# Performance work log

Measured on AMD Instinct MI355X. Metric: run time of the kernel, lower is better.

Reference implementation:

```python
import jax, jax.numpy as jnp
import numpy as np

B, D, I, H, K = 1024, 128, 64, 256, 8
HE = 2 * H  # encoder cell width (mu || log_sigma2)


def setup_inputs() -> dict:
    key = jax.random.key(0)
    ks = jax.random.split(key, 20)
    g = lambda i, shape, s=0.05: jax.random.normal(ks[i], shape, dtype=jnp.float32) * s
    return dict(
        X=g(0, (B, D, I), 1.0),
        W=jax.random.randint(ks[1], (B, D, I), 0, 2).astype(jnp.int32),
        noise=g(2, (B, H), 1.0),
        A=g(3, (D, I)),  # imputation template (learned)
        enc_Wx=g(4, (I, 4 * HE)), enc_Wh=g(5, (HE, 4 * HE)), enc_b=jnp.zeros((4 * HE,), jnp.float32),
        enc_pi=g(6, (HE,)), enc_pf=g(7, (HE,)), enc_po=g(8, (HE,)),
        dec_Wx=g(9, (I, 4 * H)), dec_Wh=g(10, (H, 4 * H)), dec_b=jnp.zeros((4 * H,), jnp.float32),
        dec_pi=g(11, (H,)), dec_pf=g(12, (H,)), dec_po=g(13, (H,)),
        out_w=g(14, (H, I)), out_b=jnp.full((I,), 0.1, jnp.float32),
        mu_c_unscaled=g(15, (K, H)), sigma2_c_unscaled=g(16, (K, H)), phi_c_unscaled=g(17, (K,)),
    )


def peephole_lstm(x_seq, Wx, Wh, b, pi, pf, po, h0, c0):
    """Keras PeepholeLSTMCell, gate order i,f,c,o. x_seq: [T,B,I] -> (hs [T,B,n], hT, cT)."""
    def step(carry, x):
        h, c = carry
        z = x @ Wx + h @ Wh + b
        zi, zf, zc, zo = jnp.split(z, 4, axis=-1)
        i = jax.nn.sigmoid(zi + pi * c)
        f = jax.nn.sigmoid(zf + pf * c)
        c_new = f * c + i * jnp.tanh(zc)
        o = jax.nn.sigmoid(zo + po * c_new)
        h_new = o * jnp.tanh(c_new)
        return (h_new, c_new), h_new
    (hT, cT), hs = jax.lax.scan(step, (h0, c0), x_seq)
    return hs, hT, cT


def reference(X, W, noise, A, enc_Wx, enc_Wh, enc_b, enc_pi, enc_pf, enc_po,
              dec_Wx, dec_Wh, dec_b, dec_pi, dec_pf, dec_po,
              out_w, out_b, mu_c_unscaled, sigma2_c_unscaled, phi_c_unscaled):
    Bn = X.shape[0]
    Wf = W.astype(X.dtype)
    X_imp = X * Wf + A * (1.0 - Wf)  # masked imputation
    # --- encode: peephole LSTM, take FINAL CELL STATE (encoder_rnn(...)[-1]) ---
    x_seq = jnp.swapaxes(X_imp, 0, 1)  # [D,B,I]
    h0 = jnp.zeros((Bn, HE), X.dtype)
    _, _, cT = peephole_lstm(x_seq, enc_Wx, enc_Wh, enc_b, enc_pi, enc_pf, enc_po, h0, h0)
    mu_tilde = cT[:, :H]
    log_sigma2_tilde = cT[:, H:]
    z = mu_tilde + jnp.exp(0.5 * log_sigma2_tilde) * noise
    # --- decode: zero inputs, initial_state = (h=0, c=z) ---
    dec_in = jnp.zeros((D, Bn, I), X.dtype)
    hs, _, _ = peephole_lstm(dec_in, dec_Wx, dec_Wh, dec_b, dec_pi, dec_pf, dec_po,
                             jnp.zeros((Bn, H), X.dtype), z)
    rnn_out = jnp.swapaxes(hs, 0, 1)  # [B,D,H]
    x_raw = rnn_out @ out_w + out_b   # [B,D,I]
    x = jax.nn.sigmoid(x_raw)
    # --- GMM parameters ---
    mu_c = mu_c_unscaled
    sigma2_c = jax.nn.softplus(sigma2_c_unscaled)
    phi_c = jax.nn.softmax(phi_c_unscaled)
    return (x, x_raw, mu_c, sigma2_c, phi_c, z, mu_tilde, log_sigma2_tilde)
```

## Files before the change

### kernel.cpp

```cpp
#include <hip/hip_runtime.h>
#include <hip/hip_bf16.h>

typedef __attribute__((ext_vector_type(4))) float f32x4;
typedef __attribute__((ext_vector_type(8))) short bf16x8;

#define NB 1024
#define ND 128
#define NI 64
#define NH 256
#define NHE 512
#define KENC 576
#define NENC 2048
#define KDEC 256
#define ESTR 584
#define DSTR 264

__device__ __forceinline__ float sigmf(float x) { return 1.0f / (1.0f + __expf(-x)); }
__device__ __forceinline__ float tanh_f(float x) { return 1.0f - 2.0f / (__expf(2.0f * x) + 1.0f); }

__device__ __forceinline__ f32x4 mfma16(bf16x8 a, bf16x8 b, f32x4 c) {
    return __builtin_amdgcn_mfma_f32_16x16x32_bf16(a, b, c, 0, 0, 0);
}

__device__ __forceinline__ void st_ull(unsigned long long* p, unsigned long long v) {
    __hip_atomic_store(p, v, __ATOMIC_RELAXED, __HIP_MEMORY_SCOPE_AGENT);
}
__device__ __forceinline__ unsigned long long ld_ull(const unsigned long long* p) {
    return __hip_atomic_load(p, __ATOMIC_RELAXED, __HIP_MEMORY_SCOPE_AGENT);
}
__device__ __forceinline__ void st_flag(int* p) {
    __hip_atomic_store(p, 1, __ATOMIC_RELAXED, __HIP_MEMORY_SCOPE_AGENT);
}

__device__ __forceinline__ void wspin(const int* flags, int n, int lane, const int* extra) {
    int g = 0;
    for (;;) {
        int v = 1;
        if (lane < n)
            v = __hip_atomic_load(flags + lane, __ATOMIC_RELAXED, __HIP_MEMORY_SCOPE_AGENT);
        else if (extra != nullptr && lane == n)
            v = __hip_atomic_load(extra, __ATOMIC_RELAXED, __HIP_MEMORY_SCOPE_AGENT);
        if (__all(v != 0)) return;
        __builtin_amdgcn_s_sleep(1);
        if (++g > (1 << 20)) return;
    }
}

__device__ __forceinline__ void quadtr(f32x4 a, int lane,
                                       float& z0, float& z1, float& z2, float& z3) {
    float x0 = a[0], x1 = a[1], x2 = a[2], x3 = a[3];
    float s0 = __shfl_xor(x0, 1), s1 = __shfl_xor(x1, 1),
          s2 = __shfl_xor(x2, 1), s3 = __shfl_xor(x3, 1);
    bool o1 = (lane & 1) != 0;
    float y0 = o1 ? s1 : x0;
    float y1 = o1 ? x1 : s0;
    float y2 = o1 ? s3 : x2;
    float y3 = o1 ? x3 : s2;
    float t0 = __shfl_xor(y0, 2), t1 = __shfl_xor(y1, 2),
          t2 = __shfl_xor(y2, 2), t3 = __shfl_xor(y3, 2);
    bool o2 = (lane & 2) != 0;
    z0 = o2 ? t2 : y0;
    z1 = o2 ? t3 : y1;
    z2 = o2 ? y2 : t0;
    z3 = o2 ? y3 : t1;
}


__global__ void pack_enc_kernel(const float* __restrict__ Wx, const float* __restrict__ Wh,
                                const float* __restrict__ bsrc,
                                __hip_bfloat16* __restrict__ Wp, float* __restrict__ bp)
{
    int n = blockIdx.y;
    int k = blockIdx.x * 256 + threadIdx.x;
    int j = n >> 2, g = n & 3;
    int col = g * NHE + j;
    if (k < KENC) {
        float v = (k < NI) ? Wx[k * NENC + col] : Wh[(k - NI) * NENC + col];
        Wp[(size_t)n * KENC + k] = __float2bfloat16(v);
    }
    if (blockIdx.x == 0 && threadIdx.x == 0) bp[n] = bsrc[col];
}

__global__ void pack_dec_kernel(const float* __restrict__ Wh, const float* __restrict__ ow,
                                const float* __restrict__ bsrc,
                                __hip_bfloat16* __restrict__ Wp, float* __restrict__ bp)
{
    int n = blockIdx.y;
    int k = threadIdx.x;
    float v;
    if (n < 1024) {
        int j = n >> 2, g = n & 3;
        int col = g * NH + j;
        v = Wh[k * 1024 + col];
        if (k == 0) bp[n] = bsrc[col];
    } else if (n < 1088) {
        v = ow[k * NI + (n - 1024)];
    } else {
        v = 0.0f;
    }
    Wp[(size_t)n * KDEC + k] = __float2bfloat16(v);
}

__global__ void pack_xb_kernel(const float* __restrict__ X, const int* __restrict__ W,
                               const float* __restrict__ A, __hip_bfloat16* __restrict__ Xb)
{
    int idx = blockIdx.x * 256 + threadIdx.x;
    int i = idx & 63;
    int t1 = idx >> 6;
    int b = t1 & 1023;
    int d = t1 >> 10;
    int src = (b * ND + d) * NI + i;
    float v = W[src] ? X[src] : A[d * NI + i];
    Xb[idx] = __float2bfloat16(v);
}

__global__ __launch_bounds__(256, 2) void enc_persist(
    const __hip_bfloat16* __restrict__ Xb,
    __hip_bfloat16* __restrict__ h0buf, __hip_bfloat16* __restrict__ h1buf,
    float* __restrict__ cenc,
    const __hip_bfloat16* __restrict__ Wp, const float* __restrict__ bp,
    const float* __restrict__ pi, const float* __restrict__ pf, const float* __restrict__ po,
    int* __restrict__ encfl)
{
    __shared__ __align__(16) unsigned short Alds[32][ESTR];
    __shared__ __align__(16) unsigned short Hlds[32][36];

    const int tid  = threadIdx.x;
    const int lane = tid & 63;
    const int wv   = tid >> 6;
    const int bm   = blockIdx.x;
    const int bn   = blockIdx.y;
    const int m0   = bm * 32;
    const int lr   = lane & 15;
    const int q    = lane >> 4;
    const int lk   = q * 8;

    bf16x8 breg[2][18];
    #pragma unroll
    for (int ni = 0; ni < 2; ++ni) {
        const __hip_bfloat16* wb = Wp + (size_t)(bn * 128 + wv * 32 + ni * 16 + lr) * KENC + lk;
        #pragma unroll
        for (int i = 0; i < 18; ++i)
            breg[ni][i] = *reinterpret_cast<const bf16x8*>(wb + i * 32);
    }

    const int u = lr >> 2;
    const int e = lane & 3;
    float4 bb[2];
    float ppi[2], ppf[2], ppo[2];
    int jl[2];
    #pragma unroll
    for (int ni = 0; ni < 2; ++ni) {
        jl[ni] = wv * 8 + ni * 4 + u;
        int jg = bn * 32 + jl[ni];
        bb[ni] = *reinterpret_cast<const float4*>(bp + 4 * jg);
        ppi[ni] = pi[jg]; ppf[ni] = pf[jg]; ppo[ni] = po[jg];
    }
    const int rowb = 4 * q + e;

    float creg[2][2] = {{0.f, 0.f}, {0.f, 0.f}};
    __hip_bfloat16* hbuf[2] = {h0buf, h1buf};

    for (int t = 0; t < ND; ++t) {
        {
            int row = tid >> 3, ch = tid & 7;
            *reinterpret_cast<bf16x8*>(&Alds[row][ch * 8]) =
                *reinterpret_cast<const bf16x8*>(Xb + ((size_t)t * NB + m0 + row) * NI + ch * 8);
        }
        __syncthreads();

        f32x4 acc[2][2];
        #pragma unroll
        for (int mi = 0; mi < 2; ++mi)
            #pragma unroll
            for (int ni = 0; ni < 2; ++ni) acc[mi][ni] = {0.f, 0.f, 0.f, 0.f};
        #pragma unroll
        for (int i = 0; i < 2; ++i) {
            bf16x8 a[2];
            #pragma unroll
            for (int mi = 0; mi < 2; ++mi)
                a[mi] = *reinterpret_cast<const bf16x8*>(&Alds[16 * mi + lr][i * 32 + lk]);
            #pragma unroll
            for (int mi = 0; mi < 2; ++mi)
                #pragma unroll
                for (int ni = 0; ni < 2; ++ni)
                    acc[mi][ni] = mfma16(a[mi], breg[ni][i], acc[mi][ni]);
        }

        if (t > 0) wspin(encfl + (size_t)(bm * ND + (t - 1)) * 16, 16, lane, nullptr);

        {
            const unsigned long long* hsrc =
                (const unsigned long long*)(hbuf[t & 1] + (size_t)m0 * NHE);
            #pragma unroll
            for (int it = 0; it < 16; ++it) {
                int idx = tid + it * 256;
                int row = idx >> 7, c8 = idx & 127;
                unsigned long long v = ld_ull(hsrc + (size_t)row * 128 + c8);
                *reinterpret_cast<unsigned long long*>(&Alds[row][64 + c8 * 4]) = v;
            }
        }
        __syncthreads();

        #pragma unroll
        for (int i = 2; i < 18; ++i) {
            bf16x8 a[2];
            #pragma unroll
            for (int mi = 0; mi < 2; ++mi)
                a[mi] = *reinterpret_cast<const bf16x8*>(&Alds[16 * mi + lr][i * 32 + lk]);
            #pragma unroll
            for (int mi = 0; mi < 2; ++mi)
                #pragma unroll
                for (int ni = 0; ni < 2; ++ni)
                    acc[mi][ni] = mfma16(a[mi], breg[ni][i], acc[mi][ni]);
        }

        #pragma unroll
        for (int mi = 0; mi < 2; ++mi) {
            #pragma unroll
            for (int ni = 0; ni < 2; ++ni) {
                float z0, z1, z2, z3;
                quadtr(acc[mi][ni], lane, z0, z1, z2, z3);
                float c_old = creg[mi][ni];
                float gi = sigmf(z0 + bb[ni].x + ppi[ni] * c_old);
                float gf = sigmf(z1 + bb[ni].y + ppf[ni] * c_old);
                float cn = gf * c_old + gi * tanh_f(z2 + bb[ni].z);
                float go = sigmf(z3 + bb[ni].w + ppo[ni] * cn);
                creg[mi][ni] = cn;
                int row = 16 * mi + rowb;
                __hip_bfloat16 hv = __float2bfloat16(go * tanh_f(cn));
                Hlds[row][jl[ni]] = reinterpret_cast<unsigned short&>(hv);
                if (t == ND - 1)
                    cenc[(size_t)(m0 + row) * NHE + bn * 32 + jl[ni]] = cn;
            }
        }
        __syncthreads();

        if (t < ND - 1) {
            {
                int row = tid >> 3, k8 = tid & 7;
                __hip_bfloat16* hdst = hbuf[(t + 1) & 1];
                unsigned long long v =
                    *reinterpret_cast<const unsigned long long*>(&Hlds[row][k8 * 4]);
                st_ull((unsigned long long*)(hdst + (size_t)(m0 + row) * NHE + bn * 32 + k8 * 4), v);
            }
            __syncthreads();
            if (tid == 0) st_flag(encfl + (size_t)(bm * ND + t) * 16 + bn);
        }
    }
}

__global__ __launch_bounds__(256, 2) void dec_persist(
    __hip_bfloat16* __restrict__ hd0, __hip_bfloat16* __restrict__ hd1,
    const float* __restrict__ zdec,
    const __hip_bfloat16* __restrict__ Wp, const float* __restrict__ bp,
    const float* __restrict__ pi, const float* __restrict__ pf, const float* __restrict__ po,
    const float* __restrict__ ob,
    float* __restrict__ ox, float* __restrict__ oxr,
    int* __restrict__ decfl, int* __restrict__ decpr)
{
    __shared__ __align__(16) unsigned short Alds[32][DSTR];
    __shared__ __align__(16) unsigned short Hlds[32][36];

    const int tid  = threadIdx.x;
    const int lane = tid & 63;
    const int wv   = tid >> 6;
    const int bm   = blockIdx.x;
    const int bn   = blockIdx.y;
    const int m0   = bm * 32;
    const int lr   = lane & 15;
    const int q    = lane >> 4;
    const int lk   = q * 8;

    __hip_bfloat16* hbuf[2] = {hd0, hd1};

    if (bn < 8) {
        bf16x8 breg[2][8];
        #pragma unroll
        for (int ni = 0; ni < 2; ++ni) {
            const __hip_bfloat16* wb = Wp + (size_t)(bn * 128 + wv * 32 + ni * 16 + lr) * KDEC + lk;
            #pragma unroll
            for (int i = 0; i < 8; ++i)
                breg[ni][i] = *reinterpret_cast<const bf16x8*>(wb + i * 32);
        }

        const int u = lr >> 2;
        const int e = lane & 3;
        float4 bb[2];
        float ppi[2], ppf[2], ppo[2];
        int jl[2];
        #pragma unroll
        for (int ni = 0; ni < 2; ++ni) {
            jl[ni] = wv * 8 + ni * 4 + u;
            int jg = bn * 32 + jl[ni];
            bb[ni] = *reinterpret_cast<const float4*>(bp + 4 * jg);
            ppi[ni] = pi[jg]; ppf[ni] = pf[jg]; ppo[ni] = po[jg];
        }
        const int rowb = 4 * q + e;

        float creg[2][2];
        #pragma unroll
        for (int mi = 0; mi < 2; ++mi)
            #pragma unroll
            for (int ni = 0; ni < 2; ++ni)
                creg[mi][ni] = zdec[(size_t)(m0 + 16 * mi + rowb) * NH + bn * 32 + jl[ni]];

        for (int t = 0; t < ND; ++t) {
            if (t >= 1) {
                const int* ex = (t >= 2) ? (decpr + bm * ND + (t - 2)) : nullptr;
                wspin(decfl + (size_t)(bm * ND + (t - 1)) * 8, 8, lane, ex);
            }

            {
                const unsigned long long* hsrc =
                    (const unsigned long long*)(hbuf[t & 1] + (size_t)m0 * NH);
                #pragma unroll
                for (int it = 0; it < 8; ++it) {
                    int idx = tid + it * 256;
                    int row = idx >> 6, c8 = idx & 63;
                    unsigned long long v = ld_ull(hsrc + (size_t)row * 64 + c8);
                    *reinterpret_cast<unsigned long long*>(&Alds[row][c8 * 4]) = v;
                }
            }
            __syncthreads();

            f32x4 acc[2][2];
            #pragma unroll
            for (int mi = 0; mi < 2; ++mi)
                #pragma unroll
                for (int ni = 0; ni < 2; ++ni) acc[mi][ni] = {0.f, 0.f, 0.f, 0.f};
            #pragma unroll
            for (int i = 0; i < 8; ++i) {
                bf16x8 a[2];
                #pragma unroll
                for (int mi = 0; mi < 2; ++mi)
                    a[mi] = *reinterpret_cast<const bf16x8*>(&Alds[16 * mi + lr][i * 32 + lk]);
                #pragma unroll
                for (int mi = 0; mi < 2; ++mi)
                    #pragma unroll
                    for (int ni = 0; ni < 2; ++ni)
                        acc[mi][ni] = mfma16(a[mi], breg[ni][i], acc[mi][ni]);
            }

            #pragma unroll
            for (int mi = 0; mi < 2; ++mi) {
                #pragma unroll
                for (int ni = 0; ni < 2; ++ni) {
                    float z0, z1, z2, z3;
                    quadtr(acc[mi][ni], lane, z0, z1, z2, z3);
                    float c_old = creg[mi][ni];
                    float gi = sigmf(z0 + bb[ni].x + ppi[ni] * c_old);
                    float gf = sigmf(z1 + bb[ni].y + ppf[ni] * c_old);
                    float cn = gf * c_old + gi * tanh_f(z2 + bb[ni].z);
                    float go = sigmf(z3 + bb[ni].w + ppo[ni] * cn);
                    creg[mi][ni] = cn;
                    int row = 16 * mi + rowb;
                    __hip_bfloat16 hv = __float2bfloat16(go * tanh_f(cn));
                    Hlds[row][jl[ni]] = reinterpret_cast<unsigned short&>(hv);
                }
            }
            __syncthreads();

            {
                int row = tid >> 3, k8 = tid & 7;
                __hip_bfloat16* hdst = hbuf[(t + 1) & 1];
                unsigned long long v =
                    *reinterpret_cast<const unsigned long long*>(&Hlds[row][k8 * 4]);
                st_ull((unsigned long long*)(hdst + (size_t)(m0 + row) * NH + bn * 32 + k8 * 4), v);
            }
            __syncthreads();
            if (tid == 0) st_flag(decfl + (size_t)(bm * ND + t) * 8 + bn);
        }
    } else {
        bf16x8 breg[8];
        const __hip_bfloat16* wb = Wp + (size_t)(1024 + wv * 16 + lr) * KDEC + lk;
        #pragma unroll
        for (int i = 0; i < 8; ++i)
            breg[i] = *reinterpret_cast<const bf16x8*>(wb + i * 32);
        const float obv = ob[wv * 16 + lr];

        for (int s = 0; s < ND; ++s) {
            wspin(decfl + (size_t)(bm * ND + s) * 8, 8, lane, nullptr);
            __syncthreads();

            {
                const unsigned long long* hsrc =
                    (const unsigned long long*)(hbuf[(s + 1) & 1] + (size_t)m0 * NH);
                #pragma unroll
                for (int it = 0; it < 8; ++it) {
                    int idx = tid + it * 256;
                    int row = idx >> 6, c8 = idx & 63;
                    unsigned long long v = ld_ull(hsrc + (size_t)row * 64 + c8);
                    *reinterpret_cast<unsigned long long*>(&Alds[row][c8 * 4]) = v;
                }
            }
            __syncthreads();
            if (tid == 0) st_flag(decpr + bm * ND + s);

            f32x4 acc[2];
            #pragma unroll
            for (int mi = 0; mi < 2; ++mi) acc[mi] = {0.f, 0.f, 0.f, 0.f};
            #pragma unroll
            for (int i = 0; i < 8; ++i) {
                bf16x8 a[2];
                #pragma unroll
                for (int mi = 0; mi < 2; ++mi)
                    a[mi] = *reinterpret_cast<const bf16x8*>(&Alds[16 * mi + lr][i * 32 + lk]);
                #pragma unroll
                for (int mi = 0; mi < 2; ++mi)
                    acc[mi] = mfma16(a[mi], breg[i], acc[mi]);
            }

            int colp = wv * 16 + lr;
            #pragma unroll
            for (int mi = 0; mi < 2; ++mi) {
                #pragma unroll
                for (int v = 0; v < 4; ++v) {
                    int row = m0 + 16 * mi + 4 * q + v;
                    float val = acc[mi][v] + obv;
                    size_t off = (size_t)row * (ND * NI) + (size_t)s * NI + colp;
                    oxr[off] = val;
                    ox[off]  = sigmf(val);
                }
            }
        }
    }
}

__global__ void mid_kernel(const float* __restrict__ cenc, const float* __restrict__ noise,
                           float* __restrict__ zdec, float* __restrict__ oz,
                           float* __restrict__ omut, float* __restrict__ olst)
{
    int idx = blockIdx.x * 256 + threadIdx.x;
    int b = idx >> 8, h = idx & 255;
    float mu = cenc[b * NHE + h];
    float ls = cenc[b * NHE + NH + h];
    float zz = mu + expf(0.5f * ls) * noise[idx];
    omut[idx] = mu;
    olst[idx] = ls;
    oz[idx]   = zz;
    zdec[idx] = zz;
}

__global__ void mix_kernel(const float* __restrict__ mu_in, const float* __restrict__ s2_in,
                           const float* __restrict__ phi_in,
                           float* __restrict__ mu_out, float* __restrict__ s2_out,
                           float* __restrict__ phi_out)
{
    int idx = blockIdx.x * 256 + threadIdx.x;
    mu_out[idx] = mu_in[idx];
    float x = s2_in[idx];
    s2_out[idx] = (x > 20.0f) ? x : log1pf(expf(x));
    if (idx == 0) {
        float m = phi_in[0];
        for (int k = 1; k < 8; ++k) m = fmaxf(m, phi_in[k]);
        float e[8], s = 0.0f;
        for (int k = 0; k < 8; ++k) { e[k] = expf(phi_in[k] - m); s += e[k]; }
        for (int k = 0; k < 8; ++k) phi_out[k] = e[k] / s;
    }
}

extern "C" void kernel_launch(void* const* d_in, const int* in_sizes, int n_in,
                              void* d_out, int out_size, void* d_ws, size_t ws_size,
                              hipStream_t stream)
{
    const float* X     = (const float*)d_in[0];
    const int*   W     = (const int*)d_in[1];
    const float* noise = (const float*)d_in[2];
    const float* A     = (const float*)d_in[3];
    const float* eWx   = (const float*)d_in[4];
    const float* eWh   = (const float*)d_in[5];
    const float* eb    = (const float*)d_in[6];
    const float* epi   = (const float*)d_in[7];
    const float* epf   = (const float*)d_in[8];
    const float* epo   = (const float*)d_in[9];
    const float* dWh   = (const float*)d_in[11];
    const float* db    = (const float*)d_in[12];
    const float* dpi   = (const float*)d_in[13];
    const float* dpf   = (const float*)d_in[14];
    const float* dpo   = (const float*)d_in[15];
    const float* ow    = (const float*)d_in[16];
    const float* ob    = (const float*)d_in[17];
    const float* muc   = (const float*)d_in[18];
    const float* s2c   = (const float*)d_in[19];
    const float* phic  = (const float*)d_in[20];

    float* out = (float*)d_out;
    float* o_x    = out;
    float* o_xraw = out + 8388608;
    float* o_muc  = out + 16777216;
    float* o_s2c  = out + 16779264;
    float* o_phic = out + 16781312;
    float* o_z    = out + 16781320;
    float* o_mut  = out + 17043464;
    float* o_lst  = out + 17305608;

    char* ws = (char*)d_ws;
    __hip_bfloat16* Wencp = (__hip_bfloat16*)(ws + 0);
    __hip_bfloat16* Wdecp = (__hip_bfloat16*)(ws + 2359296);
    float*          bencp = (float*)(ws + 2949120);
    float*          bdecp = (float*)(ws + 2957312);
    __hip_bfloat16* Xb    = (__hip_bfloat16*)(ws + 2965504);
    __hip_bfloat16* he0   = (__hip_bfloat16*)(ws + 19742720);
    __hip_bfloat16* he1   = (__hip_bfloat16*)(ws + 20791296);
    float*          cenc  = (float*)(ws + 21839872);
    __hip_bfloat16* hd0   = (__hip_bfloat16*)(ws + 23937024);
    __hip_bfloat16* hd1   = (__hip_bfloat16*)(ws + 24461312);
    float*          zdec  = (float*)(ws + 24985600);
    int*            encfl = (int*)(ws + 26034176);
    int*            decfl = (int*)(ws + 26296320);
    int*            decpr = (int*)(ws + 26427392);

    hipMemsetAsync(he0, 0, 1048576, stream);
    hipMemsetAsync(hd0, 0, 524288, stream);
    hipMemsetAsync(encfl, 0, 409600, stream);

    pack_enc_kernel<<<dim3(3, 2048), 256, 0, stream>>>(eWx, eWh, eb, Wencp, bencp);
    pack_dec_kernel<<<dim3(1, 1152), 256, 0, stream>>>(dWh, ow, db, Wdecp, bdecp);
    pack_xb_kernel<<<32768, 256, 0, stream>>>(X, W, A, Xb);

    enc_persist<<<dim3(32, 16), 256, 0, stream>>>(
        Xb, he0, he1, cenc, Wencp, bencp, epi, epf, epo, encfl);

    mid_kernel<<<1024, 256, 0, stream>>>(cenc, noise, zdec, o_z, o_mut, o_lst);
    mix_kernel<<<8, 256, 0, stream>>>(muc, s2c, phic, o_muc, o_s2c, o_phic);

    dec_persist<<<dim3(32, 9), 256, 0, stream>>>(
        hd0, hd1, zdec, Wdecp, bdecp, dpi, dpf, dpo, ob, o_x, o_xraw, decfl, decpr);
}
```

Measured before the change: 1.703 ms.

## Process four batch chunks per persistent block to shrink grid

```diff
diff --git a/kernel.cpp b/kernel.cpp
--- a/kernel.cpp
+++ b/kernel.cpp
@@ -14,6 +14,7 @@
 #define KDEC 256
 #define ESTR 584
 #define DSTR 264
+#define NCH 4
 
 __device__ __forceinline__ float sigmf(float x) { return 1.0f / (1.0f + __expf(-x)); }
 __device__ __forceinline__ float tanh_f(float x) { return 1.0f - 2.0f / (__expf(2.0f * x) + 1.0f); }
@@ -128,9 +129,8 @@
     const int tid  = threadIdx.x;
     const int lane = tid & 63;
     const int wv   = tid >> 6;
-    const int bm   = blockIdx.x;
+    const int bg   = blockIdx.x;
     const int bn   = blockIdx.y;
-    const int m0   = bm * 32;
     const int lr   = lane & 15;
     const int q    = lane >> 4;
     const int lk   = q * 8;
@@ -158,94 +158,100 @@
     }
     const int rowb = 4 * q + e;
 
-    float creg[2][2] = {{0.f, 0.f}, {0.f, 0.f}};
+    float creg[NCH][2][2] = {};
     __hip_bfloat16* hbuf[2] = {h0buf, h1buf};
 
     for (int t = 0; t < ND; ++t) {
-        {
-            int row = tid >> 3, ch = tid & 7;
-            *reinterpret_cast<bf16x8*>(&Alds[row][ch * 8]) =
-                *reinterpret_cast<const bf16x8*>(Xb + ((size_t)t * NB + m0 + row) * NI + ch * 8);
-        }
-        __syncthreads();
-
-        f32x4 acc[2][2];
         #pragma unroll
-        for (int mi = 0; mi < 2; ++mi)
-            #pragma unroll
-            for (int ni = 0; ni < 2; ++ni) acc[mi][ni] = {0.f, 0.f, 0.f, 0.f};
-        #pragma unroll
-        for (int i = 0; i < 2; ++i) {
-            bf16x8 a[2];
+        for (int ch = 0; ch < NCH; ++ch) {
+            const int bm = bg + ch * 8;
+            const int m0 = bm * 32;
+
+            {
+                int row = tid >> 3, cc = tid & 7;
+                *reinterpret_cast<bf16x8*>(&Alds[row][cc * 8]) =
+                    *reinterpret_cast<const bf16x8*>(Xb + ((size_t)t * NB + m0 + row) * NI + cc * 8);
+            }
+            __syncthreads();
+
+            f32x4 acc[2][2];
             #pragma unroll
             for (int mi = 0; mi < 2; ++mi)
-                a[mi] = *reinterpret_cast<const bf16x8*>(&Alds[16 * mi + lr][i * 32 + lk]);
-            #pragma unroll
-            for (int mi = 0; mi < 2; ++mi)
-                #pragma unroll
-                for (int ni = 0; ni < 2; ++ni)
-                    acc[mi][ni] = mfma16(a[mi], breg[ni][i], acc[mi][ni]);
-        }
-
-        if (t > 0) wspin(encfl + (size_t)(bm * ND + (t - 1)) * 16, 16, lane, nullptr);
-
-        {
-            const unsigned long long* hsrc =
-                (const unsigned long long*)(hbuf[t & 1] + (size_t)m0 * NHE);
-            #pragma unroll
-            for (int it = 0; it < 16; ++it) {
-                int idx = tid + it * 256;
-                int row = idx >> 7, c8 = idx & 127;
-                unsigned long long v = ld_ull(hsrc + (size_t)row * 128 + c8);
-                *reinterpret_cast<unsigned long long*>(&Alds[row][64 + c8 * 4]) = v;
-            }
-        }
-        __syncthreads();
-
-        #pragma unroll
-        for (int i = 2; i < 18; ++i) {
-            bf16x8 a[2];
-            #pragma unroll
-            for (int mi = 0; mi < 2; ++mi)
-                a[mi] = *reinterpret_cast<const bf16x8*>(&Alds[16 * mi + lr][i * 32 + lk]);
-            #pragma unroll
-            for (int mi = 0; mi < 2; ++mi)
-                #pragma unroll
-                for (int ni = 0; ni < 2; ++ni)
-                    acc[mi][ni] = mfma16(a[mi], breg[ni][i], acc[mi][ni]);
-        }
-
-        #pragma unroll
-        for (int mi = 0; mi < 2; ++mi) {
-            #pragma unroll
-            for (int ni = 0; ni < 2; ++ni) {
-                float z0, z1, z2, z3;
-                quadtr(acc[mi][ni], lane, z0, z1, z2, z3);
-                float c_old = creg[mi][ni];
-                float gi = sigmf(z0 + bb[ni].x + ppi[ni] * c_old);
-                float gf = sigmf(z1 + bb[ni].y + ppf[ni] * c_old);
-                float cn = gf * c_old + gi * tanh_f(z2 + bb[ni].z);
-                float go = sigmf(z3 + bb[ni].w + ppo[ni] * cn);
-                creg[mi][ni] = cn;
-                int row = 16 * mi + rowb;
-                __hip_bfloat16 hv = __float2bfloat16(go * tanh_f(cn));
-                Hlds[row][jl[ni]] = reinterpret_cast<unsigned short&>(hv);
-                if (t == ND - 1)
-                    cenc[(size_t)(m0 + row) * NHE + bn * 32 + jl[ni]] = cn;
-            }
-        }
-        __syncthreads();
-
-        if (t < ND - 1) {
+                #pragma unroll
+                for (int ni = 0; ni < 2; ++ni) acc[mi][ni] = {0.f, 0.f, 0.f, 0.f};
+            #pragma unroll
+            for (int i = 0; i < 2; ++i) {
+                bf16x8 a[2];
+                #pragma unroll
+                for (int mi = 0; mi < 2; ++mi)
+                    a[mi] = *reinterpret_cast<const bf16x8*>(&Alds[16 * mi + lr][i * 32 + lk]);
+                #pragma unroll
+                for (int mi = 0; mi < 2; ++mi)
+                    #pragma unroll
+                    for (int ni = 0; ni < 2; ++ni)
+                        acc[mi][ni] = mfma16(a[mi], breg[ni][i], acc[mi][ni]);
+            }
+
+            if (t > 0) wspin(encfl + (size_t)(bm * ND + (t - 1)) * 16, 16, lane, nullptr);
+
             {
-                int row = tid >> 3, k8 = tid & 7;
-                __hip_bfloat16* hdst = hbuf[(t + 1) & 1];
-                unsigned long long v =
-                    *reinterpret_cast<const unsigned long long*>(&Hlds[row][k8 * 4]);
-                st_ull((unsigned long long*)(hdst + (size_t)(m0 + row) * NHE + bn * 32 + k8 * 4), v);
+                const unsigned long long* hsrc =
+                    (const unsigned long long*)(hbuf[t & 1] + (size_t)m0 * NHE);
+                #pragma unroll
+                for (int it = 0; it < 16; ++it) {
+                    int idx = tid + it * 256;
+                    unsigned long long v = ld_ull(hsrc + idx);
+                    *reinterpret_cast<unsigned long long*>(
+                        &Alds[idx >> 7][64 + (idx & 127) * 4]) = v;
+                }
             }
             __syncthreads();
-            if (tid == 0) st_flag(encfl + (size_t)(bm * ND + t) * 16 + bn);
+
+            #pragma unroll
+            for (int i = 2; i < 18; ++i) {
+                bf16x8 a[2];
+                #pragma unroll
+                for (int mi = 0; mi < 2; ++mi)
+                    a[mi] = *reinterpret_cast<const bf16x8*>(&Alds[16 * mi + lr][i * 32 + lk]);
+                #pragma unroll
+                for (int mi = 0; mi < 2; ++mi)
+                    #pragma unroll
+                    for (int ni = 0; ni < 2; ++ni)
+                        acc[mi][ni] = mfma16(a[mi], breg[ni][i], acc[mi][ni]);
+            }
+
+            #pragma unroll
+            for (int mi = 0; mi < 2; ++mi) {
+                #pragma unroll
+                for (int ni = 0; ni < 2; ++ni) {
+                    float z0, z1, z2, z3;
+                    quadtr(acc[mi][ni], lane, z0, z1, z2, z3);
+                    float c_old = creg[ch][mi][ni];
+                    float gi = sigmf(z0 + bb[ni].x + ppi[ni] * c_old);
+                    float gf = sigmf(z1 + bb[ni].y + ppf[ni] * c_old);
+                    float cn = gf * c_old + gi * tanh_f(z2 + bb[ni].z);
+                    float go = sigmf(z3 + bb[ni].w + ppo[ni] * cn);
+                    creg[ch][mi][ni] = cn;
+                    int row = 16 * mi + rowb;
+                    __hip_bfloat16 hv = __float2bfloat16(go * tanh_f(cn));
+                    Hlds[row][jl[ni]] = reinterpret_cast<unsigned short&>(hv);
+                    if (t == ND - 1)
+                        cenc[(size_t)(m0 + row) * NHE + bn * 32 + jl[ni]] = cn;
+                }
+            }
+            __syncthreads();
+
+            if (t < ND - 1) {
+                {
+                    int row = tid >> 3, k8 = tid & 7;
+                    __hip_bfloat16* hdst = hbuf[(t + 1) & 1];
+                    unsigned long long v =
+                        *reinterpret_cast<const unsigned long long*>(&Hlds[row][k8 * 4]);
+                    st_ull((unsigned long long*)(hdst + (size_t)(m0 + row) * NHE + bn * 32 + k8 * 4), v);
+                }
+                __syncthreads();
+                if (tid == 0) st_flag(encfl + (size_t)(bm * ND + t) * 16 + bn);
+            }
         }
     }
 }
@@ -265,9 +271,8 @@
     const int tid  = threadIdx.x;
     const int lane = tid & 63;
     const int wv   = tid >> 6;
-    const int bm   = blockIdx.x;
+    const int bg   = blockIdx.x;
     const int bn   = blockIdx.y;
-    const int m0   = bm * 32;
     const int lr   = lane & 15;
     const int q    = lane >> 4;
     const int lk   = q * 8;
@@ -298,78 +303,88 @@
         }
         const int rowb = 4 * q + e;
 
-        float creg[2][2];
+        float creg[NCH][2][2];
         #pragma unroll
-        for (int mi = 0; mi < 2; ++mi)
-            #pragma unroll
-            for (int ni = 0; ni < 2; ++ni)
-                creg[mi][ni] = zdec[(size_t)(m0 + 16 * mi + rowb) * NH + bn * 32 + jl[ni]];
+        for (int ch = 0; ch < NCH; ++ch) {
+            int m0c = (bg + ch * 8) * 32;
+            #pragma unroll
+            for (int mi = 0; mi < 2; ++mi)
+                #pragma unroll
+                for (int ni = 0; ni < 2; ++ni)
+                    creg[ch][mi][ni] = zdec[(size_t)(m0c + 16 * mi + rowb) * NH + bn * 32 + jl[ni]];
+        }
 
         for (int t = 0; t < ND; ++t) {
-            if (t >= 1) {
-                const int* ex = (t >= 2) ? (decpr + bm * ND + (t - 2)) : nullptr;
-                wspin(decfl + (size_t)(bm * ND + (t - 1)) * 8, 8, lane, ex);
-            }
-
-            {
-                const unsigned long long* hsrc =
-                    (const unsigned long long*)(hbuf[t & 1] + (size_t)m0 * NH);
-                #pragma unroll
-                for (int it = 0; it < 8; ++it) {
-                    int idx = tid + it * 256;
-                    int row = idx >> 6, c8 = idx & 63;
-                    unsigned long long v = ld_ull(hsrc + (size_t)row * 64 + c8);
-                    *reinterpret_cast<unsigned long long*>(&Alds[row][c8 * 4]) = v;
-                }
-            }
-            __syncthreads();
-
-            f32x4 acc[2][2];
-            #pragma unroll
-            for (int mi = 0; mi < 2; ++mi)
-                #pragma unroll
-                for (int ni = 0; ni < 2; ++ni) acc[mi][ni] = {0.f, 0.f, 0.f, 0.f};
-            #pragma unroll
-            for (int i = 0; i < 8; ++i) {
-                bf16x8 a[2];
+            #pragma unroll
+            for (int ch = 0; ch < NCH; ++ch) {
+                const int bm = bg + ch * 8;
+                const int m0 = bm * 32;
+
+                if (t >= 1) {
+                    const int* ex = (t >= 2) ? (decpr + bm * ND + (t - 2)) : nullptr;
+                    wspin(decfl + (size_t)(bm * ND + (t - 1)) * 8, 8, lane, ex);
+                }
+
+                {
+                    const unsigned long long* hsrc =
+                        (const unsigned long long*)(hbuf[t & 1] + (size_t)m0 * NH);
+                    #pragma unroll
+                    for (int it = 0; it < 8; ++it) {
+                        int idx = tid + it * 256;
+                        unsigned long long v = ld_ull(hsrc + idx);
+                        *reinterpret_cast<unsigned long long*>(
+                            &Alds[idx >> 6][(idx & 63) * 4]) = v;
+                    }
+                }
+                __syncthreads();
+
+                f32x4 acc[2][2];
                 #pragma unroll
                 for (int mi = 0; mi < 2; ++mi)
-                    a[mi] = *reinterpret_cast<const bf16x8*>(&Alds[16 * mi + lr][i * 32 + lk]);
-                #pragma unroll
-                for (int mi = 0; mi < 2; ++mi)
-                    #pragma unroll
-                    for (int ni = 0; ni < 2; ++ni)
-                        acc[mi][ni] = mfma16(a[mi], breg[ni][i], acc[mi][ni]);
-            }
-
-            #pragma unroll
-            for (int mi = 0; mi < 2; ++mi) {
-                #pragma unroll
-                for (int ni = 0; ni < 2; ++ni) {
-                    float z0, z1, z2, z3;
-                    quadtr(acc[mi][ni], lane, z0, z1, z2, z3);
-                    float c_old = creg[mi][ni];
-                    float gi = sigmf(z0 + bb[ni].x + ppi[ni] * c_old);
-                    float gf = sigmf(z1 + bb[ni].y + ppf[ni] * c_old);
-                    float cn = gf * c_old + gi * tanh_f(z2 + bb[ni].z);
-                    float go = sigmf(z3 + bb[ni].w + ppo[ni] * cn);
-                    creg[mi][ni] = cn;
-                    int row = 16 * mi + rowb;
-                    __hip_bfloat16 hv = __float2bfloat16(go * tanh_f(cn));
-                    Hlds[row][jl[ni]] = reinterpret_cast<unsigned short&>(hv);
-                }
-            }
-            __syncthreads();
-
-            {
-                int row = tid >> 3, k8 = tid & 7;
-                __hip_bfloat16* hdst = hbuf[(t + 1) & 1];
-                unsigned long long v =
-                    *reinterpret_cast<const unsigned long long*>(&Hlds[row][k8 * 4]);
-                st_ull((unsigned long long*)(hdst + (size_t)(m0 + row) * NH + bn * 32 + k8 * 4), v);
-            }
-            __syncthreads();
-            if (tid == 0) st_flag(decfl + (size_t)(bm * ND + t) * 8 + bn);
+                    #pragma unroll
+                    for (int ni = 0; ni < 2; ++ni) acc[mi][ni] = {0.f, 0.f, 0.f, 0.f};
+                #pragma unroll
+                for (int i = 0; i < 8; ++i) {
+                    bf16x8 a[2];
+                    #pragma unroll
+                    for (int mi = 0; mi < 2; ++mi)
+                        a[mi] = *reinterpret_cast<const bf16x8*>(&Alds[16 * mi + lr][i * 32 + lk]);
+                    #pragma unroll
+                    for (int mi = 0; mi < 2; ++mi)
+                        #pragma unroll
+                        for (int ni = 0; ni < 2; ++ni)
+                            acc[mi][ni] = mfma16(a[mi], breg[ni][i], acc[mi][ni]);
+                }
+
+                #pragma unroll
+                for (int mi = 0; mi < 2; ++mi) {
+                    #pragma unroll
+                    for (int ni = 0; ni < 2; ++ni) {
+                        float z0, z1, z2, z3;
+                        quadtr(acc[mi][ni], lane, z0, z1, z2, z3);
+                        float c_old = creg[ch][mi][ni];
+                        float gi = sigmf(z0 + bb[ni].x + ppi[ni] * c_old);
+                        float gf = sigmf(z1 + bb[ni].y + ppf[ni] * c_old);
+                        float cn = gf * c_old + gi * tanh_f(z2 + bb[ni].z);
+                        float go = sigmf(z3 + bb[ni].w + ppo[ni] * cn);
+                        creg[ch][mi][ni] = cn;
+                        int row = 16 * mi + rowb;
+                        __hip_bfloat16 hv = __float2bfloat16(go * tanh_f(cn));
+                        Hlds[row][jl[ni]] = reinterpret_cast<unsigned short&>(hv);
+                    }
+                }
+                __syncthreads();
+
+                {
+                    int row = tid >> 3, k8 = tid & 7;
+                    __hip_bfloat16* hdst = hbuf[(t + 1) & 1];
+                    unsigned long long v =
+                        *reinterpret_cast<const unsigned long long*>(&Hlds[row][k8 * 4]);
+                    st_ull((unsigned long long*)(hdst + (size_t)(m0 + row) * NH + bn * 32 + k8 * 4), v);
+                }
+                __syncthreads();
+                if (tid == 0) st_flag(decfl + (size_t)(bm * ND + t) * 8 + bn);
+            }
         }
     } else {
         bf16x8 breg[8];
@@ -380,47 +395,53 @@
         const float obv = ob[wv * 16 + lr];
 
         for (int s = 0; s < ND; ++s) {
-            wspin(decfl + (size_t)(bm * ND + s) * 8, 8, lane, nullptr);
-            __syncthreads();
-
-            {
-                const unsigned long long* hsrc =
-                    (const unsigned long long*)(hbuf[(s + 1) & 1] + (size_t)m0 * NH);
-                #pragma unroll
-                for (int it = 0; it < 8; ++it) {
-                    int idx = tid + it * 256;
-                    int row = idx >> 6, c8 = idx & 63;
-                    unsigned long long v = ld_ull(hsrc + (size_t)row * 64 + c8);
-                    *reinterpret_cast<unsigned long long*>(&Alds[row][c8 * 4]) = v;
-                }
-            }
-            __syncthreads();
-            if (tid == 0) st_flag(decpr + bm * ND + s);
-
-            f32x4 acc[2];
-            #pragma unroll
-            for (int mi = 0; mi < 2; ++mi) acc[mi] = {0.f, 0.f, 0.f, 0.f};
-            #pragma unroll
-            for (int i = 0; i < 8; ++i) {
-                bf16x8 a[2];
-                #pragma unroll
-                for (int mi = 0; mi < 2; ++mi)
-                    a[mi] = *reinterpret_cast<const bf16x8*>(&Alds[16 * mi + lr][i * 32 + lk]);
-                #pragma unroll
-                for (int mi = 0; mi < 2; ++mi)
-                    acc[mi] = mfma16(a[mi], breg[i], acc[mi]);
-            }
-
-            int colp = wv * 16 + lr;
-            #pragma unroll
-            for (int mi = 0; mi < 2; ++mi) {
-                #pragma unroll
-                for (int v = 0; v < 4; ++v) {
-                    int row = m0 + 16 * mi + 4 * q + v;
-                    float val = acc[mi][v] + obv;
-                    size_t off = (size_t)row * (ND * NI) + (size_t)s * NI + colp;
-                    oxr[off] = val;
-                    ox[off]  = sigmf(val);
+            #pragma unroll
+            for (int ch = 0; ch < NCH; ++ch) {
+                const int bm = bg + ch * 8;
+                const int m0 = bm * 32;
+
+                wspin(decfl + (size_t)(bm * ND + s) * 8, 8, lane, nullptr);
+                __syncthreads();
+
+                {
+                    const unsigned long long* hsrc =
+                        (const unsigned long long*)(hbuf[(s + 1) & 1] + (size_t)m0 * NH);
+                    #pragma unroll
+                    for (int it = 0; it < 8; ++it) {
+                        int idx = tid + it * 256;
+                        unsigned long long v = ld_ull(hsrc + idx);
+                        *reinterpret_cast<unsigned long long*>(
+                            &Alds[idx >> 6][(idx & 63) * 4]) = v;
+                    }
+                }
+                __syncthreads();
+                if (tid == 0) st_flag(decpr + bm * ND + s);
+
+                f32x4 acc[2];
+                #pragma unroll
+                for (int mi = 0; mi < 2; ++mi) acc[mi] = {0.f, 0.f, 0.f, 0.f};
+                #pragma unroll
+                for (int i = 0; i < 8; ++i) {
+                    bf16x8 a[2];
+                    #pragma unroll
+                    for (int mi = 0; mi < 2; ++mi)
+                        a[mi] = *reinterpret_cast<const bf16x8*>(&Alds[16 * mi + lr][i * 32 + lk]);
+                    #pragma unroll
+                    for (int mi = 0; mi < 2; ++mi)
+                        acc[mi] = mfma16(a[mi], breg[i], acc[mi]);
+                }
+
+                int colp = wv * 16 + lr;
+                #pragma unroll
+                for (int mi = 0; mi < 2; ++mi) {
+                    #pragma unroll
+                    for (int v = 0; v < 4; ++v) {
+                        int row = m0 + 16 * mi + 4 * q + v;
+                        float val = acc[mi][v] + obv;
+                        size_t off = (size_t)row * (ND * NI) + (size_t)s * NI + colp;
+                        oxr[off] = val;
+                        ox[off]  = sigmf(val);
+                    }
                 }
             }
         }
@@ -508,23 +529,23 @@
     __hip_bfloat16* hd1   = (__hip_bfloat16*)(ws + 24461312);
     float*          zdec  = (float*)(ws + 24985600);
     int*            encfl = (int*)(ws + 26034176);
-    int*            decfl = (int*)(ws + 26296320);
-    int*            decpr = (int*)(ws + 26427392);
+    int*            decfl = (int*)(ws + 27082752);
+    int*            decpr = (int*)(ws + 27607040);
 
     hipMemsetAsync(he0, 0, 1048576, stream);
     hipMemsetAsync(hd0, 0, 524288, stream);
-    hipMemsetAsync(encfl, 0, 409600, stream);
+    hipMemsetAsync(encfl, 0, 1589248, stream);
 
     pack_enc_kernel<<<dim3(3, 2048), 256, 0, stream>>>(eWx, eWh, eb, Wencp, bencp);
     pack_dec_kernel<<<dim3(1, 1152), 256, 0, stream>>>(dWh, ow, db, Wdecp, bdecp);
     pack_xb_kernel<<<32768, 256, 0, stream>>>(X, W, A, Xb);
 
-    enc_persist<<<dim3(32, 16), 256, 0, stream>>>(
+    enc_persist<<<dim3(8, 16), 256, 0, stream>>>(
         Xb, he0, he1, cenc, Wencp, bencp, epi, epf, epo, encfl);
 
     mid_kernel<<<1024, 256, 0, stream>>>(cenc, noise, zdec, o_z, o_mut, o_lst);
     mix_kernel<<<8, 256, 0, stream>>>(muc, s2c, phic, o_muc, o_s2c, o_phic);
 
-    dec_persist<<<dim3(32, 9), 256, 0, stream>>>(
+    dec_persist<<<dim3(8, 9), 256, 0, stream>>>(
         hd0, hd1, zdec, Wdecp, bdecp, dpi, dpf, dpo, ob, o_x, o_xraw, decfl, decpr);
 }
```

New measurement: 5.271 ms. 209% more time.
